# Performance work log

Hardware: AMD Instinct MI355X
Metric: run time of the kernel (lower is better)

Reference implementation:

```python
import jax, jax.numpy as jnp
import numpy as np

T, D_IN, H, E = 8192, 2048, 2048, 512


def setup_inputs() -> dict:
    key = jax.random.key(0)
    k_x, k_wi, k_wh, k_wo = jax.random.split(key, 4)
    s_in = 1.0 / np.sqrt(D_IN)
    s_h = 1.0 / np.sqrt(H)
    return {
        "inputs": jax.random.normal(k_x, (T, D_IN), dtype=jnp.float32),
        "w_i": jax.random.normal(k_wi, (D_IN, 3 * H), dtype=jnp.float32) * s_in,
        "w_h": jax.random.normal(k_wh, (H, 3 * H), dtype=jnp.float32) * s_h,
        "b": jnp.zeros((3 * H,), dtype=jnp.float32),
        "w_out": jax.random.normal(k_wo, (H, E), dtype=jnp.float32) * s_h,
        "b_out": jnp.zeros((E,), dtype=jnp.float32),
    }


def reference(inputs, w_i, w_h, b, w_out, b_out):
    h_size = w_h.shape[0]
    w_h_zr = w_h[:, : 2 * h_size]   # [H, 2H]
    w_h_a = w_h[:, 2 * h_size :]    # [H, H]
    b_zr = b[: 2 * h_size]
    b_a = b[2 * h_size :]

    def step(h, x):
        gates_x = x @ w_i                       # [3H]
        zr_x = gates_x[: 2 * h_size]
        a_x = gates_x[2 * h_size :]
        zr = jax.nn.sigmoid(zr_x + h @ w_h_zr + b_zr)
        z, r = zr[:h_size], zr[h_size:]
        a = jnp.tanh(a_x + (r * h) @ w_h_a + b_a)
        h_new = (1.0 - z) * h + z * a
        return h_new, None

    h0 = jnp.zeros((h_size,), dtype=inputs.dtype)
    h_final, _ = jax.lax.scan(step, h0, inputs)
    return h_final @ w_out + b_out
```

## Files before the change

kernel.cpp:

```cpp
#include <hip/hip_runtime.h>
#include <stdint.h>

#define T_STEPS 8192
#define DIN     2048
#define HD      2048
#define G3      6144
#define EOUT    512

#define NA 128
#define NB 64
#define HP 1024
#define NREP 8
#define SPIN_MAX (1<<20)

typedef unsigned long long u64;
typedef __attribute__((ext_vector_type(8))) __bf16 bf16x8;
typedef __attribute__((ext_vector_type(8))) unsigned short u16x8;
typedef __attribute__((ext_vector_type(4))) float f32x4;

__device__ __forceinline__ uint16_t f2bf(float v){
  uint32_t x = __float_as_uint(v);
  return (uint16_t)((x + 0x7fffu + ((x >> 16) & 1u)) >> 16);
}

__device__ __forceinline__ u64 aload(const u64* p){
  return __hip_atomic_load(p, __ATOMIC_RELAXED, __HIP_MEMORY_SCOPE_AGENT);
}
__device__ __forceinline__ void astore(u64* p, u64 v){
  __hip_atomic_store(p, v, __ATOMIC_RELAXED, __HIP_MEMORY_SCOPE_AGENT);
}

__device__ __forceinline__ bf16x8 load_afrag(const float* __restrict__ w, int col, int kb){
  u16x8 r;
  #pragma unroll
  for (int j = 0; j < 8; ++j)
    r[j] = f2bf(w[(size_t)(kb + j)*G3 + col]);
  return __builtin_bit_cast(bf16x8, r);
}

__global__ __launch_bounds__(256) void gates_gemm(const float* __restrict__ A,
                                                  const float* __restrict__ B,
                                                  float* __restrict__ C){
  __shared__ float As[16*132];
  __shared__ float Bs[16*132];
  const int bm = blockIdx.x / (G3/128);
  const int bn = blockIdx.x % (G3/128);
  const int row0 = bm*128, col0 = bn*128;
  const int tid = threadIdx.x;
  const int tr = tid >> 4, tc = tid & 15;
  float acc[8][8] = {};
  for (int k0 = 0; k0 < DIN; k0 += 16){
    {
      int r = tid >> 4, c = tid & 15;
      #pragma unroll
      for (int i = 0; i < 8; ++i){
        int row = r + 16*i;
        As[c*132 + row] = A[(size_t)(row0 + row)*DIN + k0 + c];
      }
    }
    {
      int kk = tid >> 7, cc = tid & 127;
      #pragma unroll
      for (int i = 0; i < 8; ++i){
        int k = kk + 2*i;
        Bs[k*132 + cc] = B[(size_t)(k0 + k)*G3 + col0 + cc];
      }
    }
    __syncthreads();
    #pragma unroll
    for (int kk = 0; kk < 16; ++kk){
      float4 a0 = *(float4*)&As[kk*132 + 8*tr];
      float4 a1 = *(float4*)&As[kk*132 + 8*tr + 4];
      float4 b0 = *(float4*)&Bs[kk*132 + 8*tc];
      float4 b1 = *(float4*)&Bs[kk*132 + 8*tc + 4];
      float av[8] = {a0.x,a0.y,a0.z,a0.w,a1.x,a1.y,a1.z,a1.w};
      float bv[8] = {b0.x,b0.y,b0.z,b0.w,b1.x,b1.y,b1.z,b1.w};
      #pragma unroll
      for (int i = 0; i < 8; ++i)
        #pragma unroll
        for (int j = 0; j < 8; ++j)
          acc[i][j] = fmaf(av[i], bv[j], acc[i][j]);
    }
    __syncthreads();
  }
  #pragma unroll
  for (int i = 0; i < 8; ++i){
    size_t off = (size_t)(row0 + 8*tr + i)*G3 + col0 + 8*tc;
    float4 v0 = {acc[i][0],acc[i][1],acc[i][2],acc[i][3]};
    float4 v1 = {acc[i][4],acc[i][5],acc[i][6],acc[i][7]};
    *(float4*)(C + off)     = v0;
    *(float4*)(C + off + 4) = v1;
  }
}

__global__ __launch_bounds__(512) void scan_kernel(
    const float* __restrict__ gates, const float* __restrict__ w_h,
    const float* __restrict__ b,
    u64* hbuf, u64* rhbuf, u64* zbufg, float* hfinal)
{
  __shared__ uint32_t vpack[2][1024];
  __shared__ float    red[32*9];
  __shared__ float    gx[2][32];
  __shared__ float    zsl[2][32];
  __shared__ float    hloc[2][32];
  __shared__ int      dead;
  volatile int* deadp = &dead;

  const int tid  = threadIdx.x;
  const int lane = tid & 63;
  const int wid  = tid >> 6;
  const bool isA = blockIdx.x < NA;
  const int  g   = isA ? (int)blockIdx.x : (int)blockIdx.x - NA;
  const int  rep = blockIdx.x & (NREP - 1);

  int colG0, colG1;
  if (isA){ colG0 = 2048 + 16*g + (lane & 15); colG1 = 16*g + (lane & 15); }
  else    { colG0 = 4096 + 32*g + (lane & 15); colG1 = colG0 + 16; }

  bf16x8 aw0[8], aw1[8];
  {
    const int kb0 = wid*256 + ((lane >> 4) << 3);
    #pragma unroll
    for (int s = 0; s < 8; ++s){
      aw0[s] = load_afrag(w_h, colG0, kb0 + s*32);
      aw1[s] = load_afrag(w_h, colG1, kb0 + s*32);
    }
  }

  if (tid == 0) *deadp = 0;
  if (tid < 64) ((float*)hloc)[tid] = 0.f;

  int   gcol = -1;
  float bias = 0.f;
  if (isA) { if (tid < 16)      gcol = 2048 + 16*g + tid;
             else if (tid < 32) gcol = 16*g + (tid - 16); }
  else     { if (tid < 32)      gcol = 4096 + 32*g + tid; }
  if (gcol >= 0) { bias = b[gcol]; gx[0][tid] = gates[gcol] + bias; }
  __syncthreads();

  for (int t = 0; t < T_STEPS; ++t){
    const int par = t & 1;

    if (isA){
      const u64* src = hbuf + ((size_t)(rep*2 + par))*HP;
      u64 v0, v1; int spins = 0;
      const uint32_t want = (uint32_t)t;
      for(;;){
        v0 = aload(src + tid);
        v1 = aload(src + tid + 512);
        if ((uint32_t)(v0 >> 32) >= want && (uint32_t)(v1 >> 32) >= want) break;
        if (*deadp) break;
        if (++spins > SPIN_MAX){ *deadp = 1; break; }
        __builtin_amdgcn_s_sleep(1);
      }
      vpack[par][tid]       = (uint32_t)v0;
      vpack[par][tid + 512] = (uint32_t)v1;
    } else {
      const u64* src = rhbuf + ((size_t)(rep*2 + par))*HP;
      const u64* zs  = zbufg + (size_t)par*2048 + 32*g;
      const bool needz = (tid < 32);
      u64 v0, v1, vz = 0; int spins = 0;
      const uint32_t want = (uint32_t)(t + 1);
      for(;;){
        v0 = aload(src + tid);
        v1 = aload(src + tid + 512);
        if (needz) vz = aload(zs + tid);
        bool ok = (uint32_t)(v0 >> 32) >= want &&
                  (uint32_t)(v1 >> 32) >= want &&
                  (!needz || (uint32_t)(vz >> 32) >= want);
        if (ok) break;
        if (*deadp) break;
        if (++spins > SPIN_MAX){ *deadp = 1; break; }
        __builtin_amdgcn_s_sleep(1);
      }
      vpack[par][tid]       = (uint32_t)v0;
      vpack[par][tid + 512] = (uint32_t)v1;
      if (needz) zsl[par][tid] = __uint_as_float((uint32_t)vz);
    }
    __syncthreads();
    if (*deadp) break;

    {
      const uint32_t* vp = &vpack[par][wid*128];
      const int boff = (lane >> 4) << 2;
      f32x4 acc0 = {0.f,0.f,0.f,0.f}, acc1 = {0.f,0.f,0.f,0.f};
      #pragma unroll
      for (int s = 0; s < 8; ++s){
        uint4 bu = *(const uint4*)(vp + s*16 + boff);
        bf16x8 bf = __builtin_bit_cast(bf16x8, bu);
        acc0 = __builtin_amdgcn_mfma_f32_16x16x32_bf16(aw0[s], bf, acc0, 0, 0, 0);
        acc1 = __builtin_amdgcn_mfma_f32_16x16x32_bf16(aw1[s], bf, acc1, 0, 0, 0);
      }
      if ((lane & 15) == 0){
        int mb = (lane >> 4) << 2;
        #pragma unroll
        for (int r = 0; r < 4; ++r){
          red[(mb + r)*9 + wid]        = acc0[r];
          red[(16 + mb + r)*9 + wid]   = acc1[r];
        }
      }
    }
    __syncthreads();

    if (tid < 32){
      float acc = 0.f;
      #pragma unroll
      for (int w = 0; w < 8; ++w) acc += red[tid*9 + w];
      float pre = acc + gx[par][tid];

      if (isA){
        if (tid < 16){
          float r = 1.f / (1.f + __expf(-pre));
          int hcol = 16*g + tid;
          uint32_t hp = vpack[par][hcol >> 1];
          float hval = __uint_as_float((hcol & 1) ? (hp & 0xffff0000u) : (hp << 16));
          float rh = r * hval;
          float other = __shfl_xor(rh, 1);
          if (!(tid & 1)){
            u64 pv = ((u64)(uint32_t)(t + 1) << 32)
                   | ((u64)f2bf(other) << 16) | (u64)f2bf(rh);
            size_t idx = (size_t)((16*g + tid) >> 1);
            #pragma unroll
            for (int rp = 0; rp < NREP; ++rp)
              astore(rhbuf + (size_t)(rp*2 + par)*HP + idx, pv);
          }
        } else {
          float z = 1.f / (1.f + __expf(-pre));
          u64 pv = ((u64)(uint32_t)(t + 1) << 32) | (u64)__float_as_uint(z);
          astore(zbufg + (size_t)par*2048 + 16*g + (tid - 16), pv);
        }
      } else {
        float e = __expf(2.f*pre);
        float a = 1.f - 2.f/(1.f + e);
        float z = zsl[par][tid];
        float hold = hloc[par][tid];
        float hnew = hold + z*(a - hold);
        float other = __shfl_xor(hnew, 1);
        if (!(tid & 1)){
          u64 pv = ((u64)(uint32_t)(t + 1) << 32)
                 | ((u64)f2bf(other) << 16) | (u64)f2bf(hnew);
          size_t idx = (size_t)((32*g + tid) >> 1);
          #pragma unroll
          for (int rp = 0; rp < NREP; ++rp)
            astore(hbuf + (size_t)(rp*2 + ((t+1)&1))*HP + idx, pv);
        }
        hloc[par ^ 1][tid] = hnew;
      }

      if (gcol >= 0){
        int tn = (t + 1 < T_STEPS) ? t + 1 : t;
        gx[par ^ 1][tid] = gates[(size_t)tn*G3 + gcol] + bias;
      }
    }
  }

  if (!isA && tid < 32) hfinal[32*g + tid] = hloc[0][tid];
}

__global__ __launch_bounds__(1024) void out_proj(const float* __restrict__ hfin,
                                                 const float* __restrict__ w_out,
                                                 const float* __restrict__ b_out,
                                                 float* __restrict__ out){
  __shared__ float red[16][80];
  const int g  = blockIdx.x;
  const int cl = threadIdx.x & 63;
  const int kc = threadIdx.x >> 6;
  const int col = 64*g + cl;
  float acc = 0.f;
  for (int k = kc*128; k < kc*128 + 128; ++k)
    acc = fmaf(hfin[k], w_out[(size_t)k*EOUT + col], acc);
  red[kc][cl] = acc;
  __syncthreads();
  if (kc == 0){
    float s = 0.f;
    #pragma unroll
    for (int q = 0; q < 16; ++q) s += red[q][cl];
    out[col] = s + b_out[col];
  }
}

extern "C" void kernel_launch(void* const* d_in, const int* in_sizes, int n_in,
                              void* d_out, int out_size, void* d_ws, size_t ws_size,
                              hipStream_t stream) {
  const float* x     = (const float*)d_in[0];
  const float* w_i   = (const float*)d_in[1];
  const float* w_h   = (const float*)d_in[2];
  const float* b     = (const float*)d_in[3];
  const float* w_out = (const float*)d_in[4];
  const float* b_out = (const float*)d_in[5];
  float* out = (float*)d_out;

  float* gates  = (float*)d_ws;
  u64*   hbuf   = (u64*)(gates + (size_t)T_STEPS * G3);
  u64*   rhbuf  = hbuf + (size_t)NREP*2*HP;
  u64*   zbufg  = rhbuf + (size_t)NREP*2*HP;
  float* hfinal = (float*)(zbufg + 2*2048);
  (void)in_sizes; (void)n_in; (void)out_size; (void)ws_size;

  hipMemsetAsync(hbuf, 0,
                 (size_t)(NREP*2*HP + NREP*2*HP + 2*2048)*sizeof(u64), stream);

  gates_gemm<<<dim3((T_STEPS/128)*(G3/128)), dim3(256), 0, stream>>>(x, w_i, gates);

  const float* gates_c = gates;
  void* kargs[7];
  kargs[0] = (void*)&gates_c;
  kargs[1] = (void*)&w_h;
  kargs[2] = (void*)&b;
  kargs[3] = (void*)&hbuf;
  kargs[4] = (void*)&rhbuf;
  kargs[5] = (void*)&zbufg;
  kargs[6] = (void*)&hfinal;
  hipLaunchCooperativeKernel((void*)scan_kernel, dim3(NA + NB), dim3(512), kargs, 0u, stream);

  out_proj<<<dim3(EOUT/64), dim3(1024), 0, stream>>>(hfinal, w_out, b_out, out);
}
```

Baseline: 32.32 ms.

## Move z-gate into B blocks, MFMA gates GEMM, busy-poll without sleep

The scan kernel is repartitioned: A blocks now compute only the r gate, and B blocks compute the z gate from h (overlapping with waiting for r*h) before computing the candidate. This removes the separate z buffer and its cross-block handoff. The polling loop drops s_sleep and checks the dead flag only every 64 spins, cutting wake-up latency at the cost of more memory traffic. The input-gates GEMM is rewritten to use bf16 MFMA with on-the-fly conversion, which lowers precision of the precomputed gates.

```diff
diff --git a/kernel.cpp b/kernel.cpp
--- a/kernel.cpp
+++ b/kernel.cpp
@@ -7,7 +7,7 @@
 #define G3      6144
 #define EOUT    512
 
-#define NA 128
+#define NA 64
 #define NB 64
 #define HP 1024
 #define NREP 8
@@ -28,6 +28,22 @@
 }
 __device__ __forceinline__ void astore(u64* p, u64 v){
   __hip_atomic_store(p, v, __ATOMIC_RELAXED, __HIP_MEMORY_SCOPE_AGENT);
+}
+
+__device__ __forceinline__ void poll2(const u64* p0, const u64* p1, uint32_t want,
+                                      u64& r0, u64& r1, volatile int* deadp){
+  u64 a0 = aload(p0), a1 = aload(p1);
+  int spins = 0;
+  for(;;){
+    u64 b0 = aload(p0), b1 = aload(p1);
+    if ((uint32_t)(a0 >> 32) >= want && (uint32_t)(a1 >> 32) >= want) break;
+    if ((++spins & 63) == 0){
+      if (*deadp) break;
+      if (spins > SPIN_MAX){ *deadp = 1; break; }
+    }
+    a0 = b0; a1 = b1;
+  }
+  r0 = a0; r1 = a1;
 }
 
 __device__ __forceinline__ bf16x8 load_afrag(const float* __restrict__ w, int col, int kb){
@@ -38,70 +54,97 @@
   return __builtin_bit_cast(bf16x8, r);
 }
 
-__global__ __launch_bounds__(256) void gates_gemm(const float* __restrict__ A,
+__device__ __forceinline__ void mv_pass(const uint32_t* vp_base,
+                                        const bf16x8* wA, const bf16x8* wB,
+                                        float* red, int wid, int lane){
+  const uint32_t* vp = vp_base + wid*128;
+  const int boff = (lane >> 4) << 2;
+  f32x4 acc0 = {0.f,0.f,0.f,0.f}, acc1 = {0.f,0.f,0.f,0.f};
+  #pragma unroll
+  for (int s = 0; s < 8; ++s){
+    uint4 bu = *(const uint4*)(vp + s*16 + boff);
+    bf16x8 bf = __builtin_bit_cast(bf16x8, bu);
+    acc0 = __builtin_amdgcn_mfma_f32_16x16x32_bf16(wA[s], bf, acc0, 0, 0, 0);
+    acc1 = __builtin_amdgcn_mfma_f32_16x16x32_bf16(wB[s], bf, acc1, 0, 0, 0);
+  }
+  if ((lane & 15) == 0){
+    int mb = (lane >> 4) << 2;
+    #pragma unroll
+    for (int r = 0; r < 4; ++r){
+      red[(mb + r)*9 + wid]      = acc0[r];
+      red[(16 + mb + r)*9 + wid] = acc1[r];
+    }
+  }
+}
+
+__global__ __launch_bounds__(512) void gates_gemm(const float* __restrict__ A,
                                                   const float* __restrict__ B,
                                                   float* __restrict__ C){
-  __shared__ float As[16*132];
-  __shared__ float Bs[16*132];
+  __shared__ uint16_t Asb[128*40];
+  __shared__ uint16_t Bsb[128*40];
   const int bm = blockIdx.x / (G3/128);
   const int bn = blockIdx.x % (G3/128);
   const int row0 = bm*128, col0 = bn*128;
-  const int tid = threadIdx.x;
-  const int tr = tid >> 4, tc = tid & 15;
-  float acc[8][8] = {};
-  for (int k0 = 0; k0 < DIN; k0 += 16){
+  const int tid  = threadIdx.x;
+  const int lane = tid & 63, wid = tid >> 6;
+  const int wr = wid >> 2, wc = wid & 3;
+  f32x4 acc[4][2] = {};
+  for (int k0 = 0; k0 < DIN; k0 += 32){
     {
-      int r = tid >> 4, c = tid & 15;
-      #pragma unroll
-      for (int i = 0; i < 8; ++i){
-        int row = r + 16*i;
-        As[c*132 + row] = A[(size_t)(row0 + row)*DIN + k0 + c];
-      }
+      int m = tid >> 2, ks = (tid & 3) * 8;
+      const float* src = A + (size_t)(row0 + m)*DIN + k0 + ks;
+      float4 f0 = *(const float4*)src;
+      float4 f1 = *(const float4*)(src + 4);
+      u16x8 pk;
+      pk[0]=f2bf(f0.x); pk[1]=f2bf(f0.y); pk[2]=f2bf(f0.z); pk[3]=f2bf(f0.w);
+      pk[4]=f2bf(f1.x); pk[5]=f2bf(f1.y); pk[6]=f2bf(f1.z); pk[7]=f2bf(f1.w);
+      *(u16x8*)(Asb + m*40 + ks) = pk;
     }
     {
-      int kk = tid >> 7, cc = tid & 127;
-      #pragma unroll
-      for (int i = 0; i < 8; ++i){
-        int k = kk + 2*i;
-        Bs[k*132 + cc] = B[(size_t)(k0 + k)*G3 + col0 + cc];
-      }
-    }
-    __syncthreads();
-    #pragma unroll
-    for (int kk = 0; kk < 16; ++kk){
-      float4 a0 = *(float4*)&As[kk*132 + 8*tr];
-      float4 a1 = *(float4*)&As[kk*132 + 8*tr + 4];
-      float4 b0 = *(float4*)&Bs[kk*132 + 8*tc];
-      float4 b1 = *(float4*)&Bs[kk*132 + 8*tc + 4];
-      float av[8] = {a0.x,a0.y,a0.z,a0.w,a1.x,a1.y,a1.z,a1.w};
-      float bv[8] = {b0.x,b0.y,b0.z,b0.w,b1.x,b1.y,b1.z,b1.w};
+      int k = tid >> 4, n8 = tid & 15;
+      const float* src = B + (size_t)(k0 + k)*G3 + col0 + n8;
       #pragma unroll
       for (int i = 0; i < 8; ++i)
-        #pragma unroll
-        for (int j = 0; j < 8; ++j)
-          acc[i][j] = fmaf(av[i], bv[j], acc[i][j]);
+        Bsb[(n8 + 16*i)*40 + k] = f2bf(src[16*i]);
     }
     __syncthreads();
-  }
+    const int mrow = wr*64, ncol = wc*32;
+    const int fm = lane & 15, fk = (lane >> 4) * 8;
+    bf16x8 bfr[2];
+    #pragma unroll
+    for (int j = 0; j < 2; ++j)
+      bfr[j] = *(const bf16x8*)(Bsb + (ncol + j*16 + fm)*40 + fk);
+    #pragma unroll
+    for (int i = 0; i < 4; ++i){
+      bf16x8 af = *(const bf16x8*)(Asb + (mrow + i*16 + fm)*40 + fk);
+      acc[i][0] = __builtin_amdgcn_mfma_f32_16x16x32_bf16(af, bfr[0], acc[i][0], 0,0,0);
+      acc[i][1] = __builtin_amdgcn_mfma_f32_16x16x32_bf16(af, bfr[1], acc[i][1], 0,0,0);
+    }
+    __syncthreads();
+  }
+  const int mrow = row0 + wr*64, ncol = col0 + wc*32;
   #pragma unroll
-  for (int i = 0; i < 8; ++i){
-    size_t off = (size_t)(row0 + 8*tr + i)*G3 + col0 + 8*tc;
-    float4 v0 = {acc[i][0],acc[i][1],acc[i][2],acc[i][3]};
-    float4 v1 = {acc[i][4],acc[i][5],acc[i][6],acc[i][7]};
-    *(float4*)(C + off)     = v0;
-    *(float4*)(C + off + 4) = v1;
-  }
+  for (int i = 0; i < 4; ++i)
+    #pragma unroll
+    for (int j = 0; j < 2; ++j){
+      int cc = ncol + j*16 + (lane & 15);
+      int rr = mrow + i*16 + (lane >> 4)*4;
+      #pragma unroll
+      for (int q = 0; q < 4; ++q)
+        C[(size_t)(rr + q)*G3 + cc] = acc[i][j][q];
+    }
 }
 
 __global__ __launch_bounds__(512) void scan_kernel(
     const float* __restrict__ gates, const float* __restrict__ w_h,
     const float* __restrict__ b,
-    u64* hbuf, u64* rhbuf, u64* zbufg, float* hfinal)
+    u64* hbuf, u64* rhbuf, float* hfinal)
 {
-  __shared__ uint32_t vpack[2][1024];
-  __shared__ float    red[32*9];
-  __shared__ float    gx[2][32];
-  __shared__ float    zsl[2][32];
+  __shared__ uint32_t vph[2][1024];
+  __shared__ uint32_t vprh[2][1024];
+  __shared__ float    red0[32*9];
+  __shared__ float    red1[32*9];
+  __shared__ float    gx[2][64];
   __shared__ float    hloc[2][32];
   __shared__ int      dead;
   volatile int* deadp = &dead;
@@ -113,17 +156,22 @@
   const int  g   = isA ? (int)blockIdx.x : (int)blockIdx.x - NA;
   const int  rep = blockIdx.x & (NREP - 1);
 
-  int colG0, colG1;
-  if (isA){ colG0 = 2048 + 16*g + (lane & 15); colG1 = 16*g + (lane & 15); }
-  else    { colG0 = 4096 + 32*g + (lane & 15); colG1 = colG0 + 16; }
-
-  bf16x8 aw0[8], aw1[8];
+  bf16x8 w0[8], w1[8], w2[8], w3[8];
   {
     const int kb0 = wid*256 + ((lane >> 4) << 3);
+    const int c0  = isA ? (2048 + 32*g) : (32*g);
     #pragma unroll
     for (int s = 0; s < 8; ++s){
-      aw0[s] = load_afrag(w_h, colG0, kb0 + s*32);
-      aw1[s] = load_afrag(w_h, colG1, kb0 + s*32);
+      w0[s] = load_afrag(w_h, c0 + (lane & 15),      kb0 + s*32);
+      w1[s] = load_afrag(w_h, c0 + 16 + (lane & 15), kb0 + s*32);
+    }
+    if (!isA){
+      const int ca = 4096 + 32*g;
+      #pragma unroll
+      for (int s = 0; s < 8; ++s){
+        w2[s] = load_afrag(w_h, ca + (lane & 15),      kb0 + s*32);
+        w3[s] = load_afrag(w_h, ca + 16 + (lane & 15), kb0 + s*32);
+      }
     }
   }
 
@@ -132,109 +180,74 @@
 
   int   gcol = -1;
   float bias = 0.f;
-  if (isA) { if (tid < 16)      gcol = 2048 + 16*g + tid;
-             else if (tid < 32) gcol = 16*g + (tid - 16); }
-  else     { if (tid < 32)      gcol = 4096 + 32*g + tid; }
+  if (isA) { if (tid < 32) gcol = 2048 + 32*g + tid; }
+  else     { if (tid < 32)      gcol = 32*g + tid;
+             else if (tid < 64) gcol = 4096 + 32*g + (tid - 32);}
   if (gcol >= 0) { bias = b[gcol]; gx[0][tid] = gates[gcol] + bias; }
   __syncthreads();
 
   for (int t = 0; t < T_STEPS; ++t){
     const int par = t & 1;
 
-    if (isA){
+    {
       const u64* src = hbuf + ((size_t)(rep*2 + par))*HP;
-      u64 v0, v1; int spins = 0;
-      const uint32_t want = (uint32_t)t;
-      for(;;){
-        v0 = aload(src + tid);
-        v1 = aload(src + tid + 512);
-        if ((uint32_t)(v0 >> 32) >= want && (uint32_t)(v1 >> 32) >= want) break;
-        if (*deadp) break;
-        if (++spins > SPIN_MAX){ *deadp = 1; break; }
-        __builtin_amdgcn_s_sleep(1);
-      }
-      vpack[par][tid]       = (uint32_t)v0;
-      vpack[par][tid + 512] = (uint32_t)v1;
-    } else {
-      const u64* src = rhbuf + ((size_t)(rep*2 + par))*HP;
-      const u64* zs  = zbufg + (size_t)par*2048 + 32*g;
-      const bool needz = (tid < 32);
-      u64 v0, v1, vz = 0; int spins = 0;
-      const uint32_t want = (uint32_t)(t + 1);
-      for(;;){
-        v0 = aload(src + tid);
-        v1 = aload(src + tid + 512);
-        if (needz) vz = aload(zs + tid);
-        bool ok = (uint32_t)(v0 >> 32) >= want &&
-                  (uint32_t)(v1 >> 32) >= want &&
-                  (!needz || (uint32_t)(vz >> 32) >= want);
-        if (ok) break;
-        if (*deadp) break;
-        if (++spins > SPIN_MAX){ *deadp = 1; break; }
-        __builtin_amdgcn_s_sleep(1);
-      }
-      vpack[par][tid]       = (uint32_t)v0;
-      vpack[par][tid + 512] = (uint32_t)v1;
-      if (needz) zsl[par][tid] = __uint_as_float((uint32_t)vz);
+      u64 v0, v1;
+      poll2(src + tid, src + tid + 512, (uint32_t)t, v0, v1, deadp);
+      vph[par][tid]       = (uint32_t)v0;
+      vph[par][tid + 512] = (uint32_t)v1;
     }
     __syncthreads();
     if (*deadp) break;
 
-    {
-      const uint32_t* vp = &vpack[par][wid*128];
-      const int boff = (lane >> 4) << 2;
-      f32x4 acc0 = {0.f,0.f,0.f,0.f}, acc1 = {0.f,0.f,0.f,0.f};
-      #pragma unroll
-      for (int s = 0; s < 8; ++s){
-        uint4 bu = *(const uint4*)(vp + s*16 + boff);
-        bf16x8 bf = __builtin_bit_cast(bf16x8, bu);
-        acc0 = __builtin_amdgcn_mfma_f32_16x16x32_bf16(aw0[s], bf, acc0, 0, 0, 0);
-        acc1 = __builtin_amdgcn_mfma_f32_16x16x32_bf16(aw1[s], bf, acc1, 0, 0, 0);
-      }
-      if ((lane & 15) == 0){
-        int mb = (lane >> 4) << 2;
+    if (isA){
+      mv_pass(&vph[par][0], w0, w1, red0, wid, lane);
+      __syncthreads();
+      if (tid < 32){
+        float acc = 0.f;
         #pragma unroll
-        for (int r = 0; r < 4; ++r){
-          red[(mb + r)*9 + wid]        = acc0[r];
-          red[(16 + mb + r)*9 + wid]   = acc1[r];
+        for (int w = 0; w < 8; ++w) acc += red0[tid*9 + w];
+        float pre = acc + gx[par][tid];
+        float r = 1.f / (1.f + __expf(-pre));
+        int col = 32*g + tid;
+        uint32_t hp = vph[par][col >> 1];
+        float hval = __uint_as_float((col & 1) ? (hp & 0xffff0000u) : (hp << 16));
+        float rh = r * hval;
+        float other = __shfl_xor(rh, 1);
+        if (!(tid & 1)){
+          u64 pv = ((u64)(uint32_t)(t + 1) << 32)
+                 | ((u64)f2bf(other) << 16) | (u64)f2bf(rh);
+          size_t idx = (size_t)(col >> 1);
+          #pragma unroll
+          for (int rp = 0; rp < NREP; ++rp)
+            astore(rhbuf + (size_t)(rp*2 + par)*HP + idx, pv);
         }
-      }
-    }
-    __syncthreads();
-
-    if (tid < 32){
-      float acc = 0.f;
-      #pragma unroll
-      for (int w = 0; w < 8; ++w) acc += red[tid*9 + w];
-      float pre = acc + gx[par][tid];
-
-      if (isA){
-        if (tid < 16){
-          float r = 1.f / (1.f + __expf(-pre));
-          int hcol = 16*g + tid;
-          uint32_t hp = vpack[par][hcol >> 1];
-          float hval = __uint_as_float((hcol & 1) ? (hp & 0xffff0000u) : (hp << 16));
-          float rh = r * hval;
-          float other = __shfl_xor(rh, 1);
-          if (!(tid & 1)){
-            u64 pv = ((u64)(uint32_t)(t + 1) << 32)
-                   | ((u64)f2bf(other) << 16) | (u64)f2bf(rh);
-            size_t idx = (size_t)((16*g + tid) >> 1);
-            #pragma unroll
-            for (int rp = 0; rp < NREP; ++rp)
-              astore(rhbuf + (size_t)(rp*2 + par)*HP + idx, pv);
-          }
-        } else {
-          float z = 1.f / (1.f + __expf(-pre));
-          u64 pv = ((u64)(uint32_t)(t + 1) << 32) | (u64)__float_as_uint(z);
-          astore(zbufg + (size_t)par*2048 + 16*g + (tid - 16), pv);
-        }
-      } else {
-        float e = __expf(2.f*pre);
+        int tn = (t + 1 < T_STEPS) ? t + 1 : t;
+        gx[par ^ 1][tid] = gates[(size_t)tn*G3 + gcol] + bias;
+      }
+    } else {
+      mv_pass(&vph[par][0], w0, w1, red0, wid, lane);
+      {
+        const u64* src = rhbuf + ((size_t)(rep*2 + par))*HP;
+        u64 v0, v1;
+        poll2(src + tid, src + tid + 512, (uint32_t)(t + 1), v0, v1, deadp);
+        vprh[par][tid]       = (uint32_t)v0;
+        vprh[par][tid + 512] = (uint32_t)v1;
+      }
+      __syncthreads();
+      if (*deadp) break;
+      mv_pass(&vprh[par][0], w2, w3, red1, wid, lane);
+      __syncthreads();
+      if (tid < 32){
+        float zacc = 0.f, aacc = 0.f;
+        #pragma unroll
+        for (int w = 0; w < 8; ++w){ zacc += red0[tid*9 + w]; aacc += red1[tid*9 + w]; }
+        float z = 1.f / (1.f + __expf(-(zacc + gx[par][tid])));
+        float apre = aacc + gx[par][32 + tid];
+        float e = __expf(2.f*apre);
         float a = 1.f - 2.f/(1.f + e);
-        float z = zsl[par][tid];
         float hold = hloc[par][tid];
         float hnew = hold + z*(a - hold);
+        hloc[par ^ 1][tid] = hnew;
         float other = __shfl_xor(hnew, 1);
         if (!(tid & 1)){
           u64 pv = ((u64)(uint32_t)(t + 1) << 32)
@@ -244,9 +257,7 @@
           for (int rp = 0; rp < NREP; ++rp)
             astore(hbuf + (size_t)(rp*2 + ((t+1)&1))*HP + idx, pv);
         }
-        hloc[par ^ 1][tid] = hnew;
-      }
-
+      }
       if (gcol >= 0){
         int tn = (t + 1 < T_STEPS) ? t + 1 : t;
         gx[par ^ 1][tid] = gates[(size_t)tn*G3 + gcol] + bias;
@@ -293,24 +304,21 @@
   float* gates  = (float*)d_ws;
   u64*   hbuf   = (u64*)(gates + (size_t)T_STEPS * G3);
   u64*   rhbuf  = hbuf + (size_t)NREP*2*HP;
-  u64*   zbufg  = rhbuf + (size_t)NREP*2*HP;
-  float* hfinal = (float*)(zbufg + 2*2048);
+  float* hfinal = (float*)(rhbuf + (size_t)NREP*2*HP);
   (void)in_sizes; (void)n_in; (void)out_size; (void)ws_size;
 
-  hipMemsetAsync(hbuf, 0,
-                 (size_t)(NREP*2*HP + NREP*2*HP + 2*2048)*sizeof(u64), stream);
-
-  gates_gemm<<<dim3((T_STEPS/128)*(G3/128)), dim3(256), 0, stream>>>(x, w_i, gates);
+  hipMemsetAsync(hbuf, 0, (size_t)(2*NREP*2*HP)*sizeof(u64), stream);
+
+  gates_gemm<<<dim3((T_STEPS/128)*(G3/128)), dim3(512), 0, stream>>>(x, w_i, gates);
 
   const float* gates_c = gates;
-  void* kargs[7];
+  void* kargs[6];
   kargs[0] = (void*)&gates_c;
   kargs[1] = (void*)&w_h;
   kargs[2] = (void*)&b;
   kargs[3] = (void*)&hbuf;
   kargs[4] = (void*)&rhbuf;
-  kargs[5] = (void*)&zbufg;
-  kargs[6] = (void*)&hfinal;
+  kargs[5] = (void*)&hfinal;
   hipLaunchCooperativeKernel((void*)scan_kernel, dim3(NA + NB), dim3(512), kargs, 0u, stream);
 
   out_proj<<<dim3(EOUT/64), dim3(1024), 0, stream>>>(hfinal, w_out, b_out, out);
```

Measured after the change: 31.22 ms. -3.4%, faster.
